# Performance work log

Hardware: AMD Instinct MI355X
Metric: run time of the kernel (lower is better)

The kernel has to match this reference:

```python
import jax, jax.numpy as jnp
import numpy as np

B, C, H_RES, W_RES = 8, 192, 64, 64


def dwconv(x, kern, pad):
    # depthwise conv, x: (B,C,H,W), kern: (C,1,k,k)
    return jax.lax.conv_general_dilated(
        x, kern, window_strides=(1, 1), padding=[(pad, pad), (pad, pad)],
        dimension_numbers=('NCHW', 'OIHW', 'NCHW'),
        feature_group_count=x.shape[1])


def omni_shift(x, alpha, dw1, dw3, dw5):
    # OmniShift (training branch): learnable mix of identity + depthwise 1x1/3x3/5x5
    return (alpha[0] * x + alpha[1] * dwconv(x, dw1, 0)
            + alpha[2] * dwconv(x, dw3, 1) + alpha[3] * dwconv(x, dw5, 2))


def biwkv(w, u, k, v):
    # Bidirectional WKV (Vision-RWKV style):
    # out_t = (sum_{i!=t} e^{-(|t-i|-1)w + k_i} v_i + e^{u+k_t} v_t)
    #       / (sum_{i!=t} e^{-(|t-i|-1)w + k_i}       + e^{u+k_t})
    # w,u: (C,); k,v: (B,T,C). Implemented as two stable log-scaled scans.
    kT = jnp.moveaxis(k, 1, 0)  # (T,B,C)
    vT = jnp.moveaxis(v, 1, 0)
    bc = (k.shape[0], k.shape[2])
    init = (jnp.full(bc, -jnp.inf, k.dtype), jnp.zeros(bc, k.dtype), jnp.zeros(bc, k.dtype))

    def step(carry, inp):
        p, num, den = carry          # state = e^p * (num, den) over strictly-previous tokens
        kt, vt = inp
        out = (p, num, den)          # emit BEFORE absorbing token t (i != t term)
        q = jnp.maximum(p - w, kt)
        e1 = jnp.exp(p - w - q)
        e2 = jnp.exp(kt - q)
        return (q, e1 * num + e2 * vt, e1 * den + e2), out

    _, (pf, nf, df) = jax.lax.scan(step, init, (kT, vT))
    _, (pb, nb, db) = jax.lax.scan(step, init, (kT[::-1], vT[::-1]))
    pb, nb, db = pb[::-1], nb[::-1], db[::-1]

    ps = u + kT                      # self term exponent
    r = jnp.maximum(jnp.maximum(pf, pb), ps)
    ef, eb, es = jnp.exp(pf - r), jnp.exp(pb - r), jnp.exp(ps - r)
    out = (ef * nf + eb * nb + es * vT) / (ef * df + eb * db + es)
    return jnp.moveaxis(out, 0, 1)   # (B,T,C)


def setup_inputs() -> dict:
    key = jax.random.key(0)
    ks = jax.random.split(key, 12)
    s = 1.0 / np.sqrt(C)
    inp = {
        'x': jax.random.normal(ks[0], (B, C, H_RES, W_RES), jnp.float32),
        'w_key': jax.random.normal(ks[1], (C, C), jnp.float32) * s,
        'w_value': jax.random.normal(ks[2], (C, C), jnp.float32) * s,
        'w_recept': jax.random.normal(ks[3], (C, C), jnp.float32) * s,
        'w_out': jax.random.normal(ks[4], (C, C), jnp.float32) * s,
        'decay': jax.random.normal(ks[5], (C,), jnp.float32),
        'boost': jax.random.normal(ks[6], (C,), jnp.float32),
        'alpha': jax.random.normal(ks[7], (4,), jnp.float32),
        'dw1': jax.random.normal(ks[8], (C, 1, 1, 1), jnp.float32) * s,
        'dw3': jax.random.normal(ks[9], (C, 1, 3, 3), jnp.float32) * (s / 3.0),
        'dw5': jax.random.normal(ks[10], (C, 1, 5, 5), jnp.float32) * (s / 5.0),
        'H': H_RES,
        'W': W_RES,
    }
    return inp


def reference(x, w_key, w_value, w_recept, w_out, decay, boost, alpha, dw1, dw3, dw5, H, W):
    Bn, Cn = x.shape[0], x.shape[1]
    T = H * W
    xs = omni_shift(x, alpha, dw1, dw3, dw5)                 # (B,C,H,W)
    xt = jnp.transpose(xs.reshape(Bn, Cn, T), (0, 2, 1))     # (B,T,C)
    k = jnp.einsum('btc,dc->btd', xt, w_key)
    v = jnp.einsum('btc,dc->btd', xt, w_value)
    sr = jax.nn.sigmoid(jnp.einsum('btc,dc->btd', xt, w_recept))
    y = biwkv(decay / T, boost / T, k, v)                    # (B,T,C)
    y = sr * y
    y = jnp.einsum('btd,cd->btc', y, w_out)
    return jnp.transpose(y, (0, 2, 1)).reshape(Bn, Cn, H, W)
```

## Files before the change

### kernel.cpp

```cpp
#include <hip/hip_runtime.h>
#include <math.h>

#define Cn 192
#define Bn 8
#define Tn 4096
#define HW 64

typedef unsigned short u16;
typedef unsigned int u32;
typedef __attribute__((ext_vector_type(8))) __bf16 bf16x8;
typedef __attribute__((ext_vector_type(16))) float f32x16;

__device__ __forceinline__ void gload16(const void* g, void* l) {
    __builtin_amdgcn_global_load_lds(
        (const __attribute__((address_space(1))) void*)g,
        (__attribute__((address_space(3))) void*)l, 16, 0, 0);
}

__device__ __forceinline__ void split_bf16(float x, u16 &h, u16 &l) {
    u32 u = __float_as_uint(x);
    u32 uh = (u + 0x7FFFu + ((u >> 16) & 1u)) & 0xFFFF0000u;
    h = (u16)(uh >> 16);
    float r = x - __uint_as_float(uh);
    u32 ur = __float_as_uint(r);
    l = (u16)((ur + 0x7FFFu + ((ur >> 16) & 1u)) >> 16);
}

__global__ __launch_bounds__(256) void omni_kernel(const float* __restrict__ x,
                                                   const float* __restrict__ alpha,
                                                   const float* __restrict__ dw1,
                                                   const float* __restrict__ dw3,
                                                   const float* __restrict__ dw5,
                                                   const float* __restrict__ Wk,
                                                   const float* __restrict__ Wv,
                                                   const float* __restrict__ Wr,
                                                   const float* __restrict__ Wo,
                                                   u16* __restrict__ xhi,
                                                   u16* __restrict__ xlo,
                                                   u16* __restrict__ wh,
                                                   u16* __restrict__ wl) {
    const int tid = threadIdx.x;
    if (blockIdx.x >= 1536) {
        const int base = (blockIdx.x - 1536) * 768;
        #pragma unroll
        for (int jj = 0; jj < 3; ++jj) {
            int idx = base + jj * 256 + tid;
            int mat = idx / 36864;
            int off = idx - mat * 36864;
            const float* src = (mat == 0) ? Wk : (mat == 1) ? Wv : (mat == 2) ? Wr : Wo;
            u16 h, l;
            split_bf16(src[off], h, l);
            wh[idx] = h;
            wl[idx] = l;
        }
        return;
    }

    const int plane = blockIdx.x;
    const int c = plane % Cn;
    const float* xin = x + (size_t)plane * Tn;
    u16* oh = xhi + (size_t)plane * Tn;
    u16* ol = xlo + (size_t)plane * Tn;

    __shared__ float tile[68 * 68];
    __shared__ float wk[25];

    if (tid == 0) {
        const float a0 = alpha[0], a1 = alpha[1], a2 = alpha[2], a3 = alpha[3];
        #pragma unroll
        for (int j = 0; j < 25; ++j) wk[j] = a3 * dw5[c * 25 + j];
        #pragma unroll
        for (int dy = 0; dy < 3; ++dy)
            #pragma unroll
            for (int dx = 0; dx < 3; ++dx)
                wk[(dy + 1) * 5 + (dx + 1)] += a2 * dw3[c * 9 + dy * 3 + dx];
        wk[12] += a1 * dw1[c] + a0;
    }
    for (int i = tid; i < 68 * 68; i += 256) {
        int r = i / 68, cc = i - r * 68;
        int gy = r - 2, gx = cc - 2;
        float v = 0.f;
        if (gy >= 0 && gy < HW && gx >= 0 && gx < HW) v = xin[gy * HW + gx];
        tile[i] = v;
    }
    __syncthreads();

    const int py = tid >> 3;
    const int px0 = (tid & 7) << 3;

    #pragma unroll
    for (int half = 0; half < 2; ++half) {
        const int y = py + half * 32;
        float row[5][12];
        #pragma unroll
        for (int dy = 0; dy < 5; ++dy) {
            const float4* rp = (const float4*)&tile[(y + dy) * 68 + px0];
            float4 r0 = rp[0], r1 = rp[1], r2 = rp[2];
            row[dy][0] = r0.x; row[dy][1] = r0.y; row[dy][2]  = r0.z; row[dy][3]  = r0.w;
            row[dy][4] = r1.x; row[dy][5] = r1.y; row[dy][6]  = r1.z; row[dy][7]  = r1.w;
            row[dy][8] = r2.x; row[dy][9] = r2.y; row[dy][10] = r2.z; row[dy][11] = r2.w;
        }
        u32 ph[4], pl[4];
        #pragma unroll
        for (int jj = 0; jj < 8; ++jj) {
            float acc = 0.f;
            #pragma unroll
            for (int dy = 0; dy < 5; ++dy)
                #pragma unroll
                for (int dx = 0; dx < 5; ++dx)
                    acc = fmaf(row[dy][jj + dx], wk[dy * 5 + dx], acc);
            u16 h, l2;
            split_bf16(acc, h, l2);
            if (jj & 1) { ph[jj >> 1] |= ((u32)h) << 16; pl[jj >> 1] |= ((u32)l2) << 16; }
            else        { ph[jj >> 1] = h;               pl[jj >> 1] = l2; }
        }
        *(uint4*)&oh[y * 64 + px0] = make_uint4(ph[0], ph[1], ph[2], ph[3]);
        *(uint4*)&ol[y * 64 + px0] = make_uint4(pl[0], pl[1], pl[2], pl[3]);
    }
}

__global__ __launch_bounds__(256) void gemm_proj(const u16* __restrict__ wh,
                                                 const u16* __restrict__ wl,
                                                 const u16* __restrict__ Xh,
                                                 const u16* __restrict__ Xl,
                                                 float* __restrict__ O0,
                                                 float* __restrict__ O1,
                                                 float* __restrict__ O2) {
    __shared__ u16 Ah_[3 * 64 * 32], Al_[3 * 64 * 32];
    __shared__ u16 Bh_[128 * 36], Bl_[128 * 36];

    const int tid  = threadIdx.x;
    const int l    = tid & 63;
    const int wave = tid >> 6;
    const int wm   = wave >> 1, wn = wave & 1;
    const int m0   = blockIdx.y * 64;
    const int t0   = blockIdx.x * 128;
    const size_t xb = (size_t)blockIdx.z * Cn * Tn;
    const int cpair = tid & 15;
    const int toct  = tid >> 4;

    f32x16 acc[3][2];
    #pragma unroll
    for (int m = 0; m < 3; ++m)
        #pragma unroll
        for (int nf = 0; nf < 2; ++nf)
            #pragma unroll
            for (int r = 0; r < 16; ++r) acc[m][nf][r] = 0.f;

    uint4 rh0, rh1, rl0, rl1;

    auto loadB = [&](int k0) {
        size_t g = xb + (size_t)(k0 + 2 * cpair) * Tn + t0 + toct * 8;
        rh0 = *(const uint4*)&Xh[g];
        rh1 = *(const uint4*)&Xh[g + Tn];
        rl0 = *(const uint4*)&Xl[g];
        rl1 = *(const uint4*)&Xl[g + Tn];
    };
    auto writeB = [&]() {
        const u32 h0[4] = {rh0.x, rh0.y, rh0.z, rh0.w};
        const u32 h1[4] = {rh1.x, rh1.y, rh1.z, rh1.w};
        const u32 l0[4] = {rl0.x, rl0.y, rl0.z, rl0.w};
        const u32 l1[4] = {rl1.x, rl1.y, rl1.z, rl1.w};
        #pragma unroll
        for (int j = 0; j < 8; ++j) {
            int t = toct * 8 + j;
            int sh = 16 * (j & 1);
            u32 a = (h0[j >> 1] >> sh) & 0xFFFFu;
            u32 b = (h1[j >> 1] >> sh) & 0xFFFFu;
            *(u32*)&Bh_[t * 36 + 2 * cpair] = a | (b << 16);
            u32 c = (l0[j >> 1] >> sh) & 0xFFFFu;
            u32 d = (l1[j >> 1] >> sh) & 0xFFFFu;
            *(u32*)&Bl_[t * 36 + 2 * cpair] = c | (d << 16);
        }
    };
    auto stageA = [&](int k0) {
        #pragma unroll
        for (int i = 0; i < 3; ++i) {
            int idx = i * 256 + tid;
            int row = idx >> 2;
            int cb  = (idx & 3) ^ ((row >> 1) & 3);
            int grow = (row >> 6) * 192 + m0 + (row & 63);
            gload16(wh + (size_t)grow * Cn + k0 + cb * 8, Ah_ + idx * 8);
            gload16(wl + (size_t)grow * Cn + k0 + cb * 8, Al_ + idx * 8);
        }
    };
    auto compute = [&]() {
        #pragma unroll
        for (int kh = 0; kh < 2; ++kh) {
            const int cbb = kh * 2 + (l >> 5);
            bf16x8 ah[3], al[3];
            #pragma unroll
            for (int m = 0; m < 3; ++m) {
                int r = m * 64 + wm * 32 + (l & 31);
                int off = r * 32 + ((cbb ^ ((r >> 1) & 3)) << 3);
                ah[m] = *(const bf16x8*)&Ah_[off];
                al[m] = *(const bf16x8*)&Al_[off];
            }
            #pragma unroll
            for (int nf = 0; nf < 2; ++nf) {
                int t = wn * 64 + nf * 32 + (l & 31);
                int o = t * 36 + cbb * 8;
                union { uint2 q[2]; bf16x8 v; } th, tl2;
                th.q[0]  = *(const uint2*)&Bh_[o];
                th.q[1]  = *(const uint2*)&Bh_[o + 4];
                tl2.q[0] = *(const uint2*)&Bl_[o];
                tl2.q[1] = *(const uint2*)&Bl_[o + 4];
                #pragma unroll
                for (int m = 0; m < 3; ++m) {
                    acc[m][nf] = __builtin_amdgcn_mfma_f32_32x32x16_bf16(ah[m], th.v,  acc[m][nf], 0, 0, 0);
                    acc[m][nf] = __builtin_amdgcn_mfma_f32_32x32x16_bf16(ah[m], tl2.v, acc[m][nf], 0, 0, 0);
                    acc[m][nf] = __builtin_amdgcn_mfma_f32_32x32x16_bf16(al[m], th.v,  acc[m][nf], 0, 0, 0);
                }
            }
        }
    };

    loadB(0);
    stageA(0);
    writeB();
    __syncthreads();
    loadB(32);
    for (int ks = 0; ks < 6; ++ks) {
        compute();
        if (ks < 5) {
            __syncthreads();
            writeB();
            stageA((ks + 1) * 32);
            __syncthreads();
            if (ks < 4) loadB((ks + 2) * 32);
        }
    }

    float* Os[3] = {O0, O1, O2};
    #pragma unroll
    for (int m = 0; m < 3; ++m) {
        float* O = Os[m] + (size_t)blockIdx.z * Cn * Tn;
        #pragma unroll
        for (int nf = 0; nf < 2; ++nf) {
            int col = t0 + wn * 64 + nf * 32 + (l & 31);
            #pragma unroll
            for (int r = 0; r < 16; ++r) {
                int row = m0 + wm * 32 + (r & 3) + 8 * (r >> 2) + 4 * (l >> 5);
                O[(size_t)row * Tn + col] = acc[m][nf][r];
            }
        }
    }
}

__global__ __launch_bounds__(256) void wkv_stats(const float* __restrict__ kg,
                                                 const float* __restrict__ vg,
                                                 const float* __restrict__ decay,
                                                 float4* __restrict__ states) {
    const int row = blockIdx.x;
    const int d = row % Cn;
    const float* kr = kg + (size_t)row * Tn;
    const float* vr = vg + (size_t)row * Tn;

    const int tid = threadIdx.x;
    const int t0 = tid * 16;

    float kk[16], vv[16];
    #pragma unroll
    for (int j = 0; j < 16; j += 4) {
        *(float4*)&kk[j] = *(const float4*)&kr[t0 + j];
        *(float4*)&vv[j] = *(const float4*)&vr[t0 + j];
    }

    const float ww = decay[d] * (1.0f / (float)Tn);
    const float lam = expf(-ww);
    const float lam16 = expf(-16.0f * ww);

    float a[16];
    #pragma unroll
    for (int j = 0; j < 16; ++j) a[j] = expf(kk[j]);

    float SN = 0.f, SD = 0.f;
    #pragma unroll
    for (int j = 0; j < 16; ++j) { SN = fmaf(lam, SN, a[j] * vv[j]); SD = fmaf(lam, SD, a[j]); }
    float BN = 0.f, BD = 0.f;
    #pragma unroll
    for (int j = 15; j >= 0; --j) { BN = fmaf(lam, BN, a[j] * vv[j]); BD = fmaf(lam, BD, a[j]); }

    __shared__ float sN[2][256], sD[2][256];

    sN[0][tid] = SN; sD[0][tid] = SD;
    __syncthreads();
    int src = 0;
    float f = lam16;
    for (int o = 1; o < 256; o <<= 1) {
        float nN = sN[src][tid], nD = sD[src][tid];
        if (tid >= o) { nN = fmaf(f, sN[src][tid - o], nN); nD = fmaf(f, sD[src][tid - o], nD); }
        sN[src ^ 1][tid] = nN; sD[src ^ 1][tid] = nD;
        __syncthreads();
        src ^= 1; f = f * f;
    }
    const float CfN = (tid > 0) ? sN[src][tid - 1] : 0.f;
    const float CfD = (tid > 0) ? sD[src][tid - 1] : 0.f;
    __syncthreads();

    sN[0][tid] = BN; sD[0][tid] = BD;
    __syncthreads();
    src = 0; f = lam16;
    for (int o = 1; o < 256; o <<= 1) {
        float nN = sN[src][tid], nD = sD[src][tid];
        if (tid + o < 256) { nN = fmaf(f, sN[src][tid + o], nN); nD = fmaf(f, sD[src][tid + o], nD); }
        sN[src ^ 1][tid] = nN; sD[src ^ 1][tid] = nD;
        __syncthreads();
        src ^= 1; f = f * f;
    }
    const float CbN = (tid < 255) ? sN[src][tid + 1] : 0.f;
    const float CbD = (tid < 255) ? sD[src][tid + 1] : 0.f;

    const int b = row / Cn;
    states[((size_t)(b * 256 + tid)) * Cn + d] = make_float4(CfN, CfD, CbN, CbD);
}

__global__ __launch_bounds__(512) void wkv_out(const float* __restrict__ kb,
                                               const float* __restrict__ vb,
                                               const float* __restrict__ srl,
                                               const float4* __restrict__ states,
                                               const float* __restrict__ decay,
                                               const float* __restrict__ boost,
                                               const u16* __restrict__ wh,
                                               const u16* __restrict__ wl,
                                               float* __restrict__ out) {
    constexpr int ASZ = 192 * 32;
    __shared__ u16 Yh_[128 * 196], Yl_[128 * 196];
    __shared__ u16 Ah_[2 * ASZ], Al_[2 * ASZ];

    const int tid = threadIdx.x;
    const int b = blockIdx.y;
    const int t0 = blockIdx.x * 128;

    for (int pass = 0; pass < 3; ++pass) {
        const int task = pass * 512 + tid;
        const int d  = task % Cn;
        const int ch = task / Cn;
        const size_t rbase = ((size_t)b * Cn + d) * Tn + t0 + ch * 16;
        const float4 st = states[((size_t)(b * 256 + (t0 >> 4) + ch)) * Cn + d];
        const float ww = decay[d] * (1.0f / (float)Tn);
        const float lam = expf(-ww);
        const float u = boost[d] * (1.0f / (float)Tn);

        float kk[16], vv[16], sl[16];
        #pragma unroll
        for (int j = 0; j < 16; j += 4) {
            *(float4*)&kk[j] = *(const float4*)&kb[rbase + j];
            *(float4*)&vv[j] = *(const float4*)&vb[rbase + j];
            *(float4*)&sl[j] = *(const float4*)&srl[rbase + j];
        }
        float a[16];
        #pragma unroll
        for (int j = 0; j < 16; ++j) a[j] = expf(kk[j]);

        float fN[16], fD[16];
        float cN = st.x, cD = st.y;
        #pragma unroll
        for (int j = 0; j < 16; ++j) {
            fN[j] = cN; fD[j] = cD;
            cN = fmaf(lam, cN, a[j] * vv[j]);
            cD = fmaf(lam, cD, a[j]);
        }
        float bN = st.z, bD = st.w;
        #pragma unroll
        for (int j = 15; j >= 0; --j) {
            const float es = expf(u + kk[j]);
            const float y = (fN[j] + bN + es * vv[j]) / (fD[j] + bD + es);
            const float sig = 1.0f / (1.0f + expf(-sl[j]));
            u16 h, l2;
            split_bf16(sig * y, h, l2);
            const int t = ch * 16 + j;
            Yh_[t * 196 + d] = h;
            Yl_[t * 196 + d] = l2;
            bN = fmaf(lam, bN, a[j] * vv[j]);
            bD = fmaf(lam, bD, a[j]);
        }
    }
    __syncthreads();

    const int l = tid & 63;
    const int wave = tid >> 6;
    const int wm = wave >> 2;
    const int wn = wave & 3;

    f32x16 acc[3];
    #pragma unroll
    for (int mf = 0; mf < 3; ++mf)
        #pragma unroll
        for (int r = 0; r < 16; ++r) acc[mf][r] = 0.f;

    auto stageA = [&](int ks, int bf) {
        int idx = tid;
        int row = idx >> 2;
        int cb = (idx & 3) ^ ((row >> 1) & 3);
        gload16(wh + (size_t)(576 + row) * Cn + ks * 32 + cb * 8, Ah_ + bf * ASZ + idx * 8);
        gload16(wl + (size_t)(576 + row) * Cn + ks * 32 + cb * 8, Al_ + bf * ASZ + idx * 8);
        if (tid < 256) {
            idx = 512 + tid;
            row = idx >> 2;
            cb = (idx & 3) ^ ((row >> 1) & 3);
            gload16(wh + (size_t)(576 + row) * Cn + ks * 32 + cb * 8, Ah_ + bf * ASZ + idx * 8);
            gload16(wl + (size_t)(576 + row) * Cn + ks * 32 + cb * 8, Al_ + bf * ASZ + idx * 8);
        }
    };

    stageA(0, 0);
    __syncthreads();
    for (int ks = 0; ks < 6; ++ks) {
        if (ks < 5) stageA(ks + 1, (ks + 1) & 1);
        {
            const int bf = ks & 1;
            #pragma unroll
            for (int kh = 0; kh < 2; ++kh) {
                const int cbb = kh * 2 + (l >> 5);
                bf16x8 ah[3], al[3];
                #pragma unroll
                for (int mf = 0; mf < 3; ++mf) {
                    int r = wm * 96 + mf * 32 + (l & 31);
                    int off = bf * ASZ + r * 32 + ((cbb ^ ((r >> 1) & 3)) << 3);
                    ah[mf] = *(const bf16x8*)&Ah_[off];
                    al[mf] = *(const bf16x8*)&Al_[off];
                }
                const int t = wn * 32 + (l & 31);
                const int o = t * 196 + ks * 32 + cbb * 8;
                union { uint2 q[2]; bf16x8 v; } bh, bl;
                bh.q[0] = *(const uint2*)&Yh_[o];
                bh.q[1] = *(const uint2*)&Yh_[o + 4];
                bl.q[0] = *(const uint2*)&Yl_[o];
                bl.q[1] = *(const uint2*)&Yl_[o + 4];
                #pragma unroll
                for (int mf = 0; mf < 3; ++mf) {
                    acc[mf] = __builtin_amdgcn_mfma_f32_32x32x16_bf16(ah[mf], bh.v, acc[mf], 0, 0, 0);
                    acc[mf] = __builtin_amdgcn_mfma_f32_32x32x16_bf16(ah[mf], bl.v, acc[mf], 0, 0, 0);
                    acc[mf] = __builtin_amdgcn_mfma_f32_32x32x16_bf16(al[mf], bh.v, acc[mf], 0, 0, 0);
                }
            }
        }
        __syncthreads();
    }

    #pragma unroll
    for (int mf = 0; mf < 3; ++mf) {
        const int col = t0 + wn * 32 + (l & 31);
        #pragma unroll
        for (int r = 0; r < 16; ++r) {
            int row = wm * 96 + mf * 32 + (r & 3) + 8 * (r >> 2) + 4 * (l >> 5);
            out[((size_t)b * Cn + row) * Tn + col] = acc[mf][r];
        }
    }
}

extern "C" void kernel_launch(void* const* d_in, const int* in_sizes, int n_in,
                              void* d_out, int out_size, void* d_ws, size_t ws_size,
                              hipStream_t stream) {
    const float* x        = (const float*)d_in[0];
    const float* w_key    = (const float*)d_in[1];
    const float* w_value  = (const float*)d_in[2];
    const float* w_recept = (const float*)d_in[3];
    const float* w_out    = (const float*)d_in[4];
    const float* decay    = (const float*)d_in[5];
    const float* boost    = (const float*)d_in[6];
    const float* alpha    = (const float*)d_in[7];
    const float* dw1      = (const float*)d_in[8];
    const float* dw3      = (const float*)d_in[9];
    const float* dw5      = (const float*)d_in[10];

    const size_t S = (size_t)Bn * Cn * Tn;
    u16* R0 = (u16*)d_ws;
    u16* R1 = R0 + 2 * S;
    u16* R2 = R1 + 2 * S;
    u16* whp = R2 + 2 * S;
    u16* wlp = whp + 4 * 36864;

    u16* xs_hi = R0;        u16* xs_lo = R0 + S;
    float* kb  = (float*)R1;
    float* vb  = (float*)R2;
    float* srl = (float*)d_out;
    float4* states = (float4*)R0;
    float* out = (float*)d_out;

    omni_kernel<<<dim3(1536 + 192), 256, 0, stream>>>(x, alpha, dw1, dw3, dw5,
                                                      w_key, w_value, w_recept, w_out,
                                                      xs_hi, xs_lo, whp, wlp);

    gemm_proj<<<dim3(32, 3, 8), 256, 0, stream>>>(whp, wlp, xs_hi, xs_lo, kb, vb, srl);

    wkv_stats<<<dim3(Bn * Cn), 256, 0, stream>>>(kb, vb, decay, states);

    wkv_out<<<dim3(32, 8), 512, 0, stream>>>(kb, vb, srl, states, decay, boost,
                                             whp, wlp, out);
}
```

Before: 107.8 us.

## Stage k/v/sr chunks through LDS in wkv_out and alias with GEMM buffers

The WKV output phase now stages each 16-token chunk of k, v and sr for all channels into shared memory using async global-to-LDS loads, then lets 192 threads run the per-channel scans out of LDS. Previously each thread read its own strided rows directly from global memory over three passes. The staging buffers share a pool with the GEMM A tiles to keep LDS usage flat. The cost is eight serialized chunk iterations with two barriers each, and only 192 of 512 threads active during compute, so less parallelism is available to hide exp and divide latency.

```diff
diff --git a/kernel.cpp b/kernel.cpp
--- a/kernel.cpp
+++ b/kernel.cpp
@@ -326,57 +326,79 @@
                                                float* __restrict__ out) {
     constexpr int ASZ = 192 * 32;
     __shared__ u16 Yh_[128 * 196], Yl_[128 * 196];
-    __shared__ u16 Ah_[2 * ASZ], Al_[2 * ASZ];
+    __shared__ __align__(16) char pool_[49152];
+    u16* Ah_ = (u16*)pool_;
+    u16* Al_ = (u16*)(pool_ + 24576);
+    float* kS = (float*)pool_;
+    float* vS = (float*)(pool_ + 12288);
+    float* sS = (float*)(pool_ + 24576);
 
     const int tid = threadIdx.x;
     const int b = blockIdx.y;
     const int t0 = blockIdx.x * 128;
 
-    for (int pass = 0; pass < 3; ++pass) {
-        const int task = pass * 512 + tid;
-        const int d  = task % Cn;
-        const int ch = task / Cn;
-        const size_t rbase = ((size_t)b * Cn + d) * Tn + t0 + ch * 16;
-        const float4 st = states[((size_t)(b * 256 + (t0 >> 4) + ch)) * Cn + d];
-        const float ww = decay[d] * (1.0f / (float)Tn);
-        const float lam = expf(-ww);
-        const float u = boost[d] * (1.0f / (float)Tn);
-
-        float kk[16], vv[16], sl[16];
-        #pragma unroll
-        for (int j = 0; j < 16; j += 4) {
-            *(float4*)&kk[j] = *(const float4*)&kb[rbase + j];
-            *(float4*)&vv[j] = *(const float4*)&vb[rbase + j];
-            *(float4*)&sl[j] = *(const float4*)&srl[rbase + j];
-        }
-        float a[16];
-        #pragma unroll
-        for (int j = 0; j < 16; ++j) a[j] = expf(kk[j]);
-
-        float fN[16], fD[16];
-        float cN = st.x, cD = st.y;
-        #pragma unroll
-        for (int j = 0; j < 16; ++j) {
-            fN[j] = cN; fD[j] = cD;
-            cN = fmaf(lam, cN, a[j] * vv[j]);
-            cD = fmaf(lam, cD, a[j]);
-        }
-        float bN = st.z, bD = st.w;
-        #pragma unroll
-        for (int j = 15; j >= 0; --j) {
-            const float es = expf(u + kk[j]);
-            const float y = (fN[j] + bN + es * vv[j]) / (fD[j] + bD + es);
-            const float sig = 1.0f / (1.0f + expf(-sl[j]));
-            u16 h, l2;
-            split_bf16(sig * y, h, l2);
-            const int t = ch * 16 + j;
-            Yh_[t * 196 + d] = h;
-            Yl_[t * 196 + d] = l2;
-            bN = fmaf(lam, bN, a[j] * vv[j]);
-            bD = fmaf(lam, bD, a[j]);
-        }
-    }
-    __syncthreads();
+    const int dm = (tid < Cn) ? tid : 0;
+    const float lamM = expf(-decay[dm] * (1.0f / (float)Tn));
+    const float uM   = boost[dm] * (1.0f / (float)Tn);
+
+    auto stage1 = [&](const float* g, float* s) {
+        int r = tid;
+        gload16(g + (size_t)(r >> 2) * Tn + (r & 3) * 4, (char*)s + r * 16);
+        if (tid < 256) {
+            r = 512 + tid;
+            gload16(g + (size_t)(r >> 2) * Tn + (r & 3) * 4, (char*)s + r * 16);
+        }
+    };
+
+    const float* kc0 = kb  + (size_t)b * Cn * Tn + t0;
+    const float* vc0 = vb  + (size_t)b * Cn * Tn + t0;
+    const float* sc0 = srl + (size_t)b * Cn * Tn + t0;
+
+    for (int ch = 0; ch < 8; ++ch) {
+        stage1(kc0 + ch * 16, kS);
+        stage1(vc0 + ch * 16, vS);
+        stage1(sc0 + ch * 16, sS);
+        __syncthreads();
+
+        if (tid < Cn) {
+            const int d = tid;
+            const float4 st = states[((size_t)(b * 256 + (t0 >> 4) + ch)) * Cn + d];
+            float kk[16], vv[16], sl[16];
+            #pragma unroll
+            for (int j = 0; j < 16; j += 4) {
+                *(float4*)&kk[j] = *(const float4*)&kS[d * 16 + j];
+                *(float4*)&vv[j] = *(const float4*)&vS[d * 16 + j];
+                *(float4*)&sl[j] = *(const float4*)&sS[d * 16 + j];
+            }
+            float a[16];
+            #pragma unroll
+            for (int j = 0; j < 16; ++j) a[j] = expf(kk[j]);
+
+            float fN[16], fD[16];
+            float cN = st.x, cD = st.y;
+            #pragma unroll
+            for (int j = 0; j < 16; ++j) {
+                fN[j] = cN; fD[j] = cD;
+                cN = fmaf(lamM, cN, a[j] * vv[j]);
+                cD = fmaf(lamM, cD, a[j]);
+            }
+            float bN = st.z, bD = st.w;
+            #pragma unroll
+            for (int j = 15; j >= 0; --j) {
+                const float es = expf(uM + kk[j]);
+                const float y = (fN[j] + bN + es * vv[j]) / (fD[j] + bD + es);
+                const float sig = 1.0f / (1.0f + expf(-sl[j]));
+                u16 h, l2;
+                split_bf16(sig * y, h, l2);
+                const int t = ch * 16 + j;
+                Yh_[t * 196 + d] = h;
+                Yl_[t * 196 + d] = l2;
+                bN = fmaf(lamM, bN, a[j] * vv[j]);
+                bD = fmaf(lamM, bD, a[j]);
+            }
+        }
+        __syncthreads();
+    }
 
     const int l = tid & 63;
     const int wave = tid >> 6;
```

Result: slower. 123.5 us (+14.6%).
